# Performance work log

Hardware: AMD Instinct MI355X
Metric: run time of the kernel (lower is better)

## Reference

```python
import jax, jax.numpy as jnp
import numpy as np
from jax import lax
from jax.scipy.special import logsumexp

TEMP_MIN, TEMP_MAX = 0.1, 1.0
B, I, J, C = 2, 128, 512, 256


def setup_inputs() -> dict:
    key = jax.random.key(0)
    k1, k2, k3 = jax.random.split(key, 3)
    return {
        "text_embeddings": jax.random.normal(k1, (B, I, C), dtype=jnp.float32),
        "mel_embeddings": jax.random.normal(k2, (B, J, C), dtype=jnp.float32),
        "text_mask": jnp.ones((B, I), dtype=jnp.float32),
        "mel_mask": jnp.ones((B, J), dtype=jnp.float32),
        "noise": jax.random.gumbel(k3, (B, I, J), dtype=jnp.float32),  # -log(-log(U))
        "temperature_ratio": jnp.float32(0.5),
    }


def _cond_prob(energy, text_mask, mel_mask, direction):
    # energy: [B, I, J]; returns [B, I, J, K] log conditional probs (normalized over axis 2)
    b, i, j = energy.shape
    if direction == "alpha":
        k = j
        tri = jnp.arange(j)[:, None] >= jnp.arange(k)[None, :]  # triu(ones(J,J)).T layout -> j >= k
        mel_k = mel_mask
    else:  # beta
        k = j - 1
        tri = jnp.arange(j)[:, None] <= jnp.arange(k)[None, :]  # tril(ones(J-1,J)).T layout -> j <= k
        mel_k = mel_mask[:, :k]
    valid = (
        (text_mask[:, :, None, None] * mel_mask[:, None, :, None] * mel_k[:, None, None, :]) > 0
    ) & tri[None, None]
    e4 = jnp.where(valid, energy[..., None], -jnp.inf)  # [B,I,J,K]
    e4 = e4 - logsumexp(e4, axis=2, keepdims=True)
    return jnp.where(valid, e4, jnp.asarray(-10.0, energy.dtype))


def reference(text_embeddings, mel_embeddings, text_mask, mel_mask, noise, temperature_ratio):
    b, i_len, ct = text_embeddings.shape
    j_len, cm = mel_embeddings.shape[1], mel_embeddings.shape[2]
    ninf = jnp.asarray(-jnp.inf, text_embeddings.dtype)

    energy = jnp.einsum("bic,bjc->bij", text_embeddings, mel_embeddings) / np.sqrt(ct * cm)
    temperature = TEMP_MIN + (TEMP_MAX - TEMP_MIN) * temperature_ratio
    energy = (energy + noise) / temperature

    cpa = _cond_prob(energy, text_mask, mel_mask, "alpha")  # [B,I,J,J]
    cpb = _cond_prob(energy, text_mask, mel_mask, "beta")   # [B,I,J,J-1]

    # forward (alpha) recursion over text dim: alpha[:, i, j+1] = LSE_k(alpha[:, i-1, k] + cpa[:, i-1, j, k])
    init_a = jnp.full((b, j_len + 1), -jnp.inf, energy.dtype).at[:, 0].set(0.0)

    def astep(carry, cpa_i):  # carry [B, J+1], cpa_i [B, J, J]
        row = logsumexp(carry[:, None, :-1] + cpa_i, axis=2)  # [B, J]
        new = jnp.concatenate([jnp.full((b, 1), -jnp.inf, energy.dtype), row], axis=1)
        return new, row

    _, arows = lax.scan(astep, init_a, jnp.swapaxes(cpa, 0, 1))
    alpha = jnp.swapaxes(arows, 0, 1)  # [B, I, J] == alpha[:, 1:, 1:]

    # backward (beta) recursion: beta[:, i, j] = LSE_k(beta[:, i+1, k+1] + cpb[:, i, j, k])
    init_b = jnp.full((b, j_len), -jnp.inf, energy.dtype).at[:, -1].set(0.0)

    def bstep(carry, cpb_i):  # carry [B, J], cpb_i [B, J, J-1]
        row = logsumexp(carry[:, None, 1:] + cpb_i, axis=2)
        return row, row

    _, brows = lax.scan(bstep, init_b, jnp.flip(jnp.swapaxes(cpb[:, : i_len - 1], 0, 1), axis=0))
    beta = jnp.concatenate([jnp.flip(brows, axis=0), init_b[None]], axis=0)
    beta = jnp.swapaxes(beta, 0, 1)  # [B, I, J]

    gamma = alpha + beta
    gmask = (text_mask[:, :, None] * mel_mask[:, None, :]) > 0
    gamma = jnp.where(gmask, gamma, ninf)
    gamma = jnp.where(gmask, gamma - logsumexp(gamma, axis=1, keepdims=True), ninf)

    expanded = jnp.einsum("bij,bic->bjc", jnp.exp(gamma), text_embeddings)
    expanded = expanded * mel_mask[:, :, None]
    return gamma, expanded
```

## Files before the change

kernel.cpp:

```cpp
#include <hip/hip_runtime.h>
#include <math.h>

#define BB 2
#define II 128
#define JJ 512
#define CC 256
#define NEL (BB*II*JJ)
#define NINF (-INFINITY)
#define K10 4.5399929762484854e-5f

template<int CTRL, int RM = 0xf, int BM = 0xf, bool BC = true>
__device__ __forceinline__ float dppf(float x) {
    return __int_as_float(__builtin_amdgcn_update_dpp(
        0, __float_as_int(x), CTRL, RM, BM, BC));
}
__device__ __forceinline__ float wscan_incl(float x) {
    x += dppf<0x111>(x);
    x += dppf<0x112>(x);
    x += dppf<0x114>(x);
    x += dppf<0x118>(x);
    x += dppf<0x142, 0xa>(x);
    x += dppf<0x143, 0xc>(x);
    return x;
}
__device__ __forceinline__ float lane_shr1(float x) { return dppf<0x138>(x); }
__device__ __forceinline__ float bcast63(float x) {
    return __int_as_float(__builtin_amdgcn_readlane(__float_as_int(x), 63));
}

__device__ __forceinline__ void tree_prefix8(const float x[8], float P[8]) {
    float t[8];
    t[0] = x[0];
    #pragma unroll
    for (int q = 1; q < 8; ++q) t[q] = x[q] + x[q-1];
    float u[8];
    u[0] = t[0]; u[1] = t[1];
    #pragma unroll
    for (int q = 2; q < 8; ++q) u[q] = t[q] + t[q-2];
    P[0] = u[0]; P[1] = u[1]; P[2] = u[2]; P[3] = u[3];
    #pragma unroll
    for (int q = 4; q < 8; ++q) P[q] = u[q] + u[q-4];
}

__device__ __forceinline__ void loadrow8(const float* __restrict__ p, float v[8]) {
    float4 a = *reinterpret_cast<const float4*>(p);
    float4 b = *reinterpret_cast<const float4*>(p + 4);
    v[0]=a.x; v[1]=a.y; v[2]=a.z; v[3]=a.w;
    v[4]=b.x; v[5]=b.y; v[6]=b.z; v[7]=b.w;
}
__device__ __forceinline__ void loadrow8_rev(const float* __restrict__ row, int lane, float v[8]) {
    float t[8];
    loadrow8(row + 504 - 8 * lane, t);
    #pragma unroll
    for (int q = 0; q < 8; ++q) v[q] = t[7 - q];
}
__device__ __forceinline__ void storerow8(float* __restrict__ p, const float v[8]) {
    *reinterpret_cast<float4*>(p)     = make_float4(v[0],v[1],v[2],v[3]);
    *reinterpret_cast<float4*>(p + 4) = make_float4(v[4],v[5],v[6],v[7]);
}

__global__ __launch_bounds__(256) void energy_kernel(
        const float* __restrict__ text, const float* __restrict__ mel,
        const float* __restrict__ noise, const float* __restrict__ ratio,
        float* __restrict__ e) {
    __shared__ float melS[64][65];
    __shared__ float texS[8][65];
    int b  = blockIdx.x;
    int i0 = blockIdx.y * 8;
    int j0 = blockIdx.z * 64;
    int t = threadIdx.x;
    int jj = t & 63, ig = t >> 6;
    float acc0 = 0.f, acc1 = 0.f;
    for (int cc = 0; cc < CC; cc += 64) {
        #pragma unroll
        for (int k = 0; k < 4; ++k) {
            int idx = t + k * 256;
            int row = idx >> 4, seg = idx & 15;
            float4 v = *reinterpret_cast<const float4*>(
                mel + (size_t)(b * JJ + j0 + row) * CC + cc + seg * 4);
            melS[row][seg*4+0] = v.x; melS[row][seg*4+1] = v.y;
            melS[row][seg*4+2] = v.z; melS[row][seg*4+3] = v.w;
        }
        if (t < 128) {
            int row = t >> 4, seg = t & 15;
            float4 v = *reinterpret_cast<const float4*>(
                text + (size_t)(b * II + i0 + row) * CC + cc + seg * 4);
            texS[row][seg*4+0] = v.x; texS[row][seg*4+1] = v.y;
            texS[row][seg*4+2] = v.z; texS[row][seg*4+3] = v.w;
        }
        __syncthreads();
        #pragma unroll 8
        for (int c = 0; c < 64; ++c) {
            float m = melS[jj][c];
            acc0 = fmaf(m, texS[ig*2+0][c], acc0);
            acc1 = fmaf(m, texS[ig*2+1][c], acc1);
        }
        __syncthreads();
    }
    float temp = 0.1f + 0.9f * ratio[0];
    float rtmp = 1.0f / temp;
    int r0 = (b * II + i0 + ig*2 + 0) * JJ + j0 + jj;
    int r1 = (b * II + i0 + ig*2 + 1) * JJ + j0 + jj;
    e[r0] = (acc0 * (1.0f/256.0f) + noise[r0]) * rtmp;
    e[r1] = (acc1 * (1.0f/256.0f) + noise[r1]) * rtmp;
}

__global__ __launch_bounds__(64) void dscan_kernel(
        const float* __restrict__ e, float* __restrict__ Ee,
        float* __restrict__ Wa, float* __restrict__ Wb) {
    int row = blockIdx.x;
    int lane = threadIdx.x;
    float v[8];
    loadrow8(e + row * JJ + lane * 8, v);
    float m = v[0];
    #pragma unroll
    for (int q = 1; q < 8; ++q) m = fmaxf(m, v[q]);
    #pragma unroll
    for (int d = 1; d < 64; d <<= 1) m = fmaxf(m, __shfl_xor(m, d, 64));
    float x[8];
    #pragma unroll
    for (int q = 0; q < 8; ++q) x[q] = __expf(v[q] - m);
    storerow8(Ee + row * JJ + lane * 8, x);
    float run = 0.f, P[8];
    #pragma unroll
    for (int q = 0; q < 8; ++q) { run += x[q]; P[q] = run; }
    float sc = wscan_incl(run);
    float cp = lane_shr1(sc);
    float run2 = 0.f, S[8];
    #pragma unroll
    for (int q = 7; q >= 0; --q) { run2 += x[q]; S[q] = run2; }
    float sd = run2;
    #pragma unroll
    for (int d = 1; d < 64; d <<= 1) { float o = __shfl_down(sd, d, 64); sd += (lane + d < 64) ? o : 0.0f; }
    float cs = __shfl_down(sd, 1, 64); if (lane == 63) cs = 0.f;
    float wa[8], wb[8];
    #pragma unroll
    for (int q = 0; q < 8; ++q) {
        wa[q] = 1.0f / (S[q] + cs);
        wb[q] = 1.0f / (P[q] + cp);
    }
    storerow8(Wa + row * JJ + lane * 8, wa);
    storerow8(Wb + row * JJ + lane * 8, wb);
}

template<bool NORM>
__device__ __forceinline__ void astep(
    int i, int lane, int off, bool pf,
    float (&p)[8], float& c,
    float (&CE)[8], float (&CW)[8],
    float (&LE)[8], float (&LW)[8],
    const float* __restrict__ EeB, const float* __restrict__ WaB,
    float* __restrict__ paB, float* __restrict__ caB)
{
    storerow8(paB + (size_t)(i - 1) * JJ + off, p);
    if (lane == 0) caB[i - 1] = c;
    __builtin_amdgcn_sched_barrier(0);
    if (pf) {
        loadrow8(EeB + (size_t)(i + 3) * JJ + off, LE);
        loadrow8(WaB + (size_t)(i + 3) * JJ + off, LW);
    }
    __builtin_amdgcn_sched_barrier(0);

    float pup = lane_shr1(p[7]);
    float y[8];
    y[0] = pup * CW[0];
    #pragma unroll
    for (int q = 1; q < 8; ++q) y[q] = p[q-1] * CW[q];
    float zz[8];
    #pragma unroll
    for (int q = 0; q < 7; ++q) zz[q] = p[q];
    zz[7] = (lane == 63) ? 0.0f : p[7];
    float Y[8], Z[8];
    tree_prefix8(y, Y);
    tree_prefix8(zz, Z);
    float sy = wscan_incl(Y[7]);
    float sz = wscan_incl(Z[7]);
    float oy = lane_shr1(sy);
    float oz = lane_shr1(sz);
    float T  = bcast63(sz);
    #pragma unroll
    for (int q = 0; q < 8; ++q) {
        float S1 = oy + Y[q];
        float S2 = fmaxf(T - (oz + Z[q]) + zz[q], 0.0f);
        p[q] = fmaf(CE[q], S1, K10 * S2);
    }
    if (NORM) {
        float Tc = fmaxf(T, 1e-30f);
        float rT = __builtin_amdgcn_rcpf(Tc);
        c += __logf(Tc);
        #pragma unroll
        for (int q = 0; q < 8; ++q) p[q] *= rT;
    }
}

template<bool NORM>
__device__ __forceinline__ void bstep(
    int i, int lane, int off, bool pf,
    float (&p)[8], float& c,
    float (&CE)[8], float (&CW)[8],
    float (&LE)[8], float (&LW)[8],
    const float* __restrict__ EeB, const float* __restrict__ WbB,
    float* __restrict__ pbB, float* __restrict__ cbB)
{
    storerow8(pbB + (size_t)(i + 1) * JJ + off, p);
    if (lane == 0) cbB[i + 1] = c;
    __builtin_amdgcn_sched_barrier(0);
    if (pf) {
        loadrow8_rev(EeB + (size_t)(i - 3) * JJ, lane, LE);
        loadrow8_rev(WbB + (size_t)(i - 3) * JJ, lane, LW);
    }
    __builtin_amdgcn_sched_barrier(0);

    float pup = lane_shr1(p[7]);
    float pn[8];
    pn[0] = pup;
    #pragma unroll
    for (int q = 1; q < 8; ++q) pn[q] = p[q-1];
    float w[8];
    #pragma unroll
    for (int q = 0; q < 8; ++q) w[q] = pn[q] * CW[q];
    float W[8], N[8];
    tree_prefix8(w, W);
    tree_prefix8(pn, N);
    float sw = wscan_incl(W[7]);
    float sn = wscan_incl(N[7]);
    float ow = lane_shr1(sw);
    float on = lane_shr1(sn);
    float T  = bcast63(sn);
    #pragma unroll
    for (int q = 0; q < 8; ++q) {
        float QA = ow + W[q];
        float QB = fmaxf(T - (on + N[q]), 0.0f);
        p[q] = fmaf(CE[q], QA, K10 * QB);
    }
    if (NORM) {
        float Tc = fmaxf(T, 1e-30f);
        float rT = __builtin_amdgcn_rcpf(Tc);
        c += __logf(Tc);
        #pragma unroll
        for (int q = 0; q < 8; ++q) p[q] *= rT;
    }
}

__global__ __launch_bounds__(64) void scan_ab_kernel(
        const float* __restrict__ Ee, const float* __restrict__ Wa,
        const float* __restrict__ Wb,
        float* __restrict__ pa, float* __restrict__ pb,
        float* __restrict__ ca, float* __restrict__ cb) {
    int b = blockIdx.x >> 1, dir = blockIdx.x & 1;
    int lane = threadIdx.x, off = lane * 8;
    size_t base = (size_t)b * II * JJ;
    float p[8], c = 0.0f;
    float B0e[8], B0w[8], B1e[8], B1w[8], B2e[8], B2w[8], B3e[8], B3w[8];

    if (dir == 0) {
        const float* EeB = Ee + base; const float* WaB = Wa + base;
        float* paB = pa + base; float* caB = ca + b * II;
        loadrow8(EeB + (size_t)1*JJ + off, B1e); loadrow8(WaB + (size_t)1*JJ + off, B1w);
        loadrow8(EeB + (size_t)2*JJ + off, B2e); loadrow8(WaB + (size_t)2*JJ + off, B2w);
        loadrow8(EeB + (size_t)3*JJ + off, B3e); loadrow8(WaB + (size_t)3*JJ + off, B3w);
        float e0[8];
        loadrow8(EeB + off, e0);
        float wa00 = WaB[0];
        #pragma unroll
        for (int q = 0; q < 8; ++q) p[q] = e0[q] * wa00;
        int i = 1;
        #pragma unroll 1
        for (; i + 3 <= II - 1; i += 4) {
            astep<true >(i,   lane, off, i+3 < II, p, c, B1e,B1w, B0e,B0w, EeB,WaB,paB,caB);
            astep<false>(i+1, lane, off, i+4 < II, p, c, B2e,B2w, B1e,B1w, EeB,WaB,paB,caB);
            astep<false>(i+2, lane, off, i+5 < II, p, c, B3e,B3w, B2e,B2w, EeB,WaB,paB,caB);
            astep<false>(i+3, lane, off, i+6 < II, p, c, B0e,B0w, B3e,B3w, EeB,WaB,paB,caB);
        }
        astep<true >(125, lane, off, false, p, c, B1e,B1w, B0e,B0w, EeB,WaB,paB,caB);
        astep<false>(126, lane, off, false, p, c, B2e,B2w, B1e,B1w, EeB,WaB,paB,caB);
        astep<false>(127, lane, off, false, p, c, B3e,B3w, B2e,B2w, EeB,WaB,paB,caB);
        storerow8(paB + (size_t)127 * JJ + off, p);
        if (lane == 0) caB[127] = c;
    } else {
        const float* EeB = Ee + base; const float* WbB = Wb + base;
        float* pbB = pb + base; float* cbB = cb + b * II;
        loadrow8_rev(EeB + (size_t)126*JJ, lane, B2e); loadrow8_rev(WbB + (size_t)126*JJ, lane, B2w);
        loadrow8_rev(EeB + (size_t)125*JJ, lane, B1e); loadrow8_rev(WbB + (size_t)125*JJ, lane, B1w);
        loadrow8_rev(EeB + (size_t)124*JJ, lane, B0e); loadrow8_rev(WbB + (size_t)124*JJ, lane, B0w);
        #pragma unroll
        for (int q = 0; q < 8; ++q) p[q] = 0.0f;
        p[0] = (lane == 0) ? 1.0f : 0.0f;
        int i = II - 2;
        #pragma unroll 1
        for (; i - 3 >= 0; i -= 4) {
            bstep<true >(i,   lane, off, i-3 >= 0, p, c, B2e,B2w, B3e,B3w, EeB,WbB,pbB,cbB);
            bstep<false>(i-1, lane, off, i-4 >= 0, p, c, B1e,B1w, B2e,B2w, EeB,WbB,pbB,cbB);
            bstep<false>(i-2, lane, off, i-5 >= 0, p, c, B0e,B0w, B1e,B1w, EeB,WbB,pbB,cbB);
            bstep<false>(i-3, lane, off, i-6 >= 0, p, c, B3e,B3w, B0e,B0w, EeB,WbB,pbB,cbB);
        }
        bstep<true >(2, lane, off, false, p, c, B2e,B2w, B3e,B3w, EeB,WbB,pbB,cbB);
        bstep<false>(1, lane, off, false, p, c, B1e,B1w, B2e,B2w, EeB,WbB,pbB,cbB);
        bstep<false>(0, lane, off, false, p, c, B0e,B0w, B1e,B1w, EeB,WbB,pbB,cbB);
        storerow8(pbB + off, p);
        if (lane == 0) cbB[0] = c;
    }
}

__global__ __launch_bounds__(256) void gamma_expand_kernel(
        const float* __restrict__ pa, const float* __restrict__ pb,
        const float* __restrict__ ca, const float* __restrict__ cb,
        const float* __restrict__ text, const float* __restrict__ mmask,
        float* __restrict__ gamma_out, float* __restrict__ expanded) {
    __shared__ float wt[II][9];
    __shared__ float Ei[II];
    __shared__ float red[8][33];
    int b   = blockIdx.x >> 6;
    int jj0 = (blockIdx.x & 63) * 8;
    int t = threadIdx.x;
    int q = t & 7, ic = t >> 3;

    if (t < II) Ei[t] = ca[b*II + t] + cb[b*II + t];
    __syncthreads();
    float maxc = Ei[0];
    #pragma unroll 16
    for (int i = 1; i < II; ++i) maxc = fmaxf(maxc, Ei[i]);
    __syncthreads();
    if (t < II) Ei[t] = __expf(Ei[t] - maxc);
    __syncthreads();

    size_t idx0  = (size_t)b * II * JJ + jj0 + q;
    size_t idx0r = (size_t)b * II * JJ + (JJ - 1 - jj0 - q);
    float d = 0.f;
    #pragma unroll
    for (int k = 0; k < 4; ++k) {
        int i = ic * 4 + k;
        float P = pa[idx0 + (size_t)i * JJ] * pb[idx0r + (size_t)i * JJ] * Ei[i];
        wt[i][q] = P;
        d += P;
    }
    red[q][ic] = d;
    __syncthreads();
    if (t < 8) {
        float s = 0.f;
        #pragma unroll
        for (int k = 0; k < 32; ++k) s += red[t][k];
        red[t][32] = 1.0f / fmaxf(s, 1e-37f);
    }
    __syncthreads();
    float rD = red[q][32];
    #pragma unroll
    for (int k = 0; k < 4; ++k) {
        int i = ic * 4 + k;
        float P = wt[i][q] * rD;
        wt[i][q] = P;
        gamma_out[idx0 + (size_t)i * JJ] = fmaxf(__logf(P), -1e30f);
    }
    __syncthreads();

    float acc[8] = {0,0,0,0,0,0,0,0};
    const float* txb = text + (size_t)b * II * CC + t;
    #pragma unroll 4
    for (int i = 0; i < II; ++i) {
        float tv = txb[(size_t)i * CC];
        #pragma unroll
        for (int qq = 0; qq < 8; ++qq) acc[qq] = fmaf(wt[i][qq], tv, acc[qq]);
    }
    #pragma unroll
    for (int qq = 0; qq < 8; ++qq) {
        expanded[(size_t)(b * JJ + jj0 + qq) * CC + t] =
            acc[qq] * mmask[b * JJ + jj0 + qq];
    }
}

extern "C" void kernel_launch(void* const* d_in, const int* in_sizes, int n_in,
                              void* d_out, int out_size, void* d_ws, size_t ws_size,
                              hipStream_t stream) {
    const float* text  = (const float*)d_in[0];
    const float* mel   = (const float*)d_in[1];
    const float* mmask = (const float*)d_in[3];
    const float* noise = (const float*)d_in[4];
    const float* ratio = (const float*)d_in[5];
    float* gamma_out = (float*)d_out;
    float* expanded  = (float*)d_out + NEL;

    float* ws = (float*)d_ws;
    float* Ee = ws;
    float* Wa = ws +   NEL;
    float* Wb = ws + 2*NEL;
    float* pa = ws + 3*NEL;
    float* pb = ws + 4*NEL;
    float* ca = ws + 5*NEL;
    float* cb = ws + 5*NEL + BB*II;
    float* e  = pa;

    hipLaunchKernelGGL(energy_kernel, dim3(BB, II/8, JJ/64), dim3(256), 0, stream,
                       text, mel, noise, ratio, e);
    hipLaunchKernelGGL(dscan_kernel, dim3(BB*II), dim3(64), 0, stream, e, Ee, Wa, Wb);
    hipLaunchKernelGGL(scan_ab_kernel, dim3(BB*2), dim3(64), 0, stream,
                       Ee, Wa, Wb, pa, pb, ca, cb);
    hipLaunchKernelGGL(gamma_expand_kernel, dim3(BB*64), dim3(256), 0, stream,
                       pa, pb, ca, cb, text, mmask, gamma_out, expanded);
}
```

Baseline: 141.8 us.

## Spread alpha/beta scan rows across 8 waves with LDS cross-wave prefix

The sequential alpha/beta recursion kernel moves from one 64-lane wave holding 8 elements per lane to a 512-thread block with one element per thread. Each step does an in-wave DPP scan, then combines the 8 wave totals through a small double-buffered LDS array behind one barrier per step. Prefetch depth grows to 8 rows, issued as hand-written asm loads with explicit vmcnt waits, and the normalisation constants are staged in LDS. The aim is to shorten the serial per-step latency by spreading work over more lanes. In exchange every one of the 127 steps now pays an LDS round trip and a workgroup barrier.

New measurement: 156.7 us. +10.5%, slower.

```diff
diff --git a/kernel.cpp b/kernel.cpp
--- a/kernel.cpp
+++ b/kernel.cpp
@@ -8,6 +8,8 @@
 #define NEL (BB*II*JJ)
 #define NINF (-INFINITY)
 #define K10 4.5399929762484854e-5f
+
+typedef float f32x4 __attribute__((ext_vector_type(4)));
 
 template<int CTRL, int RM = 0xf, int BM = 0xf, bool BC = true>
 __device__ __forceinline__ float dppf(float x) {
@@ -24,9 +26,6 @@
     return x;
 }
 __device__ __forceinline__ float lane_shr1(float x) { return dppf<0x138>(x); }
-__device__ __forceinline__ float bcast63(float x) {
-    return __int_as_float(__builtin_amdgcn_readlane(__float_as_int(x), 63));
-}
 
 __device__ __forceinline__ void tree_prefix8(const float x[8], float P[8]) {
     float t[8];
@@ -42,21 +41,30 @@
     for (int q = 4; q < 8; ++q) P[q] = u[q] + u[q-4];
 }
 
-__device__ __forceinline__ void loadrow8(const float* __restrict__ p, float v[8]) {
+__device__ __forceinline__ void loadrow8(const float* p, float v[8]) {
     float4 a = *reinterpret_cast<const float4*>(p);
     float4 b = *reinterpret_cast<const float4*>(p + 4);
     v[0]=a.x; v[1]=a.y; v[2]=a.z; v[3]=a.w;
     v[4]=b.x; v[5]=b.y; v[6]=b.z; v[7]=b.w;
 }
-__device__ __forceinline__ void loadrow8_rev(const float* __restrict__ row, int lane, float v[8]) {
-    float t[8];
-    loadrow8(row + 504 - 8 * lane, t);
-    #pragma unroll
-    for (int q = 0; q < 8; ++q) v[q] = t[7 - q];
-}
 __device__ __forceinline__ void storerow8(float* __restrict__ p, const float v[8]) {
     *reinterpret_cast<float4*>(p)     = make_float4(v[0],v[1],v[2],v[3]);
     *reinterpret_cast<float4*>(p + 4) = make_float4(v[4],v[5],v[6],v[7]);
+}
+
+__device__ __forceinline__ void aload1(float &d, const float* p) {
+    asm volatile("global_load_dword %0, %1, off" : "=&v"(d) : "v"(p) : "memory");
+}
+__device__ __forceinline__ void astore1(float d, float* p) {
+    asm volatile("global_store_dword %1, %0, off" :: "v"(d), "v"(p) : "memory");
+}
+template<int N> __device__ __forceinline__ void waitcnt_vm() {
+    asm volatile("s_waitcnt vmcnt(%0)" :: "i"(N) : "memory");
+}
+__device__ __forceinline__ void lgkm0_barrier() {
+    asm volatile("s_waitcnt lgkmcnt(0)" ::: "memory");
+    __builtin_amdgcn_s_barrier();
+    __builtin_amdgcn_sched_barrier(0);
 }
 
 __global__ __launch_bounds__(256) void energy_kernel(
@@ -143,162 +151,200 @@
     storerow8(Wb + row * JJ + lane * 8, wb);
 }
 
-template<bool NORM>
-__device__ __forceinline__ void astep(
-    int i, int lane, int off, bool pf,
-    float (&p)[8], float& c,
-    float (&CE)[8], float (&CW)[8],
-    float (&LE)[8], float (&LW)[8],
+
+template<bool NORM, int VM, bool PF, int PTY>
+__device__ __forceinline__ void astep8(int i, int t, int w, int lane,
+    float pin, float &pout, float &c, float &Be, float &Bw,
     const float* __restrict__ EeB, const float* __restrict__ WaB,
-    float* __restrict__ paB, float* __restrict__ caB)
+    float* __restrict__ paB, f32x4 (*ldsX)[8], float* ldsC)
 {
-    storerow8(paB + (size_t)(i - 1) * JJ + off, p);
-    if (lane == 0) caB[i - 1] = c;
+    astore1(pin, paB + (size_t)(i - 1) * JJ + t);
+    if (t == 0) ldsC[i - 1] = c;
+    waitcnt_vm<VM>();
     __builtin_amdgcn_sched_barrier(0);
-    if (pf) {
-        loadrow8(EeB + (size_t)(i + 3) * JJ + off, LE);
-        loadrow8(WaB + (size_t)(i + 3) * JJ + off, LW);
-    }
-    __builtin_amdgcn_sched_barrier(0);
-
-    float pup = lane_shr1(p[7]);
-    float y[8];
-    y[0] = pup * CW[0];
-    #pragma unroll
-    for (int q = 1; q < 8; ++q) y[q] = p[q-1] * CW[q];
-    float zz[8];
-    #pragma unroll
-    for (int q = 0; q < 7; ++q) zz[q] = p[q];
-    zz[7] = (lane == 63) ? 0.0f : p[7];
-    float Y[8], Z[8];
-    tree_prefix8(y, Y);
-    tree_prefix8(zz, Z);
-    float sy = wscan_incl(Y[7]);
-    float sz = wscan_incl(Z[7]);
-    float oy = lane_shr1(sy);
-    float oz = lane_shr1(sz);
-    float T  = bcast63(sz);
-    #pragma unroll
-    for (int q = 0; q < 8; ++q) {
-        float S1 = oy + Y[q];
-        float S2 = fmaxf(T - (oz + Z[q]) + zz[q], 0.0f);
-        p[q] = fmaf(CE[q], S1, K10 * S2);
-    }
+    float CE = Be, CW = Bw;
+    if (PF) { aload1(Be, EeB + (size_t)(i + 8) * JJ + t);
+              aload1(Bw, WaB + (size_t)(i + 8) * JJ + t); }
+    float zz   = (t == JJ - 1) ? 0.0f : pin;
+    float y_in = lane_shr1(pin) * CW;
+    float Yl_in = wscan_incl(y_in);
+    float Zl    = wscan_incl(zz);
+    float cw0 = __int_as_float(__builtin_amdgcn_readlane(__float_as_int(CW), 0));
+    if (lane == 63) { f32x4 xv = {pin, Yl_in, Zl, cw0}; ldsX[PTY][w] = xv; }
+    lgkm0_barrier();
+    float offY = 0.f, offZ = 0.f, T = 0.f, prevP = 0.f, pupw = 0.f;
+    #pragma unroll
+    for (int v = 0; v < 8; ++v) {
+        f32x4 xv = ldsX[PTY][v];
+        float pup_v = prevP;
+        float tY = fmaf(pup_v, xv[3], xv[1]);
+        float tZ = xv[2];
+        if (v < w)  { offY += tY; offZ += tZ; }
+        if (v == w) pupw = pup_v;
+        T += tZ;
+        prevP = xv[0];
+    }
+    float S1 = offY + Yl_in + pupw * cw0;
+    float S2 = fmaxf(T - (offZ + Zl) + zz, 0.0f);
+    pout = fmaf(CE, S1, K10 * S2);
     if (NORM) {
         float Tc = fmaxf(T, 1e-30f);
         float rT = __builtin_amdgcn_rcpf(Tc);
         c += __logf(Tc);
-        #pragma unroll
-        for (int q = 0; q < 8; ++q) p[q] *= rT;
-    }
-}
-
-template<bool NORM>
-__device__ __forceinline__ void bstep(
-    int i, int lane, int off, bool pf,
-    float (&p)[8], float& c,
-    float (&CE)[8], float (&CW)[8],
-    float (&LE)[8], float (&LW)[8],
+        pout *= rT;
+    }
+}
+
+template<bool NORM, int VM, bool PF, int PTY>
+__device__ __forceinline__ void bstep8(int i, int t, int w, int lane,
+    float pin, float &pout, float &c, float &Be, float &Bw,
     const float* __restrict__ EeB, const float* __restrict__ WbB,
-    float* __restrict__ pbB, float* __restrict__ cbB)
+    float* __restrict__ pbB, f32x4 (*ldsX)[8], float* ldsC)
 {
-    storerow8(pbB + (size_t)(i + 1) * JJ + off, p);
-    if (lane == 0) cbB[i + 1] = c;
+    astore1(pin, pbB + (size_t)(i + 1) * JJ + t);
+    if (t == 0) ldsC[i + 1] = c;
+    waitcnt_vm<VM>();
     __builtin_amdgcn_sched_barrier(0);
-    if (pf) {
-        loadrow8_rev(EeB + (size_t)(i - 3) * JJ, lane, LE);
-        loadrow8_rev(WbB + (size_t)(i - 3) * JJ, lane, LW);
-    }
-    __builtin_amdgcn_sched_barrier(0);
-
-    float pup = lane_shr1(p[7]);
-    float pn[8];
-    pn[0] = pup;
-    #pragma unroll
-    for (int q = 1; q < 8; ++q) pn[q] = p[q-1];
-    float w[8];
-    #pragma unroll
-    for (int q = 0; q < 8; ++q) w[q] = pn[q] * CW[q];
-    float W[8], N[8];
-    tree_prefix8(w, W);
-    tree_prefix8(pn, N);
-    float sw = wscan_incl(W[7]);
-    float sn = wscan_incl(N[7]);
-    float ow = lane_shr1(sw);
-    float on = lane_shr1(sn);
-    float T  = bcast63(sn);
-    #pragma unroll
-    for (int q = 0; q < 8; ++q) {
-        float QA = ow + W[q];
-        float QB = fmaxf(T - (on + N[q]), 0.0f);
-        p[q] = fmaf(CE[q], QA, K10 * QB);
-    }
+    float CE = Be, CW = Bw;
+    if (PF) { aload1(Be, EeB + (size_t)(i - 8) * JJ + (JJ - 1 - t));
+              aload1(Bw, WbB + (size_t)(i - 8) * JJ + (JJ - 1 - t)); }
+    float pn_in = lane_shr1(pin);
+    float w_in  = pn_in * CW;
+    float Wl_in = wscan_incl(w_in);
+    float Nl_in = wscan_incl(pn_in);
+    float cw0 = __int_as_float(__builtin_amdgcn_readlane(__float_as_int(CW), 0));
+    if (lane == 63) { f32x4 xv = {pin, Wl_in, Nl_in, cw0}; ldsX[PTY][w] = xv; }
+    lgkm0_barrier();
+    float offW = 0.f, offN = 0.f, T = 0.f, prevP = 0.f, pupw = 0.f;
+    #pragma unroll
+    for (int v = 0; v < 8; ++v) {
+        f32x4 xv = ldsX[PTY][v];
+        float pup_v = prevP;
+        float tW = fmaf(pup_v, xv[3], xv[1]);
+        float tN = xv[2] + pup_v;
+        if (v < w)  { offW += tW; offN += tN; }
+        if (v == w) pupw = pup_v;
+        T += tN;
+        prevP = xv[0];
+    }
+    float QA = offW + Wl_in + pupw * cw0;
+    float Nl = Nl_in + pupw;
+    float QB = fmaxf(T - (offN + Nl), 0.0f);
+    pout = fmaf(CE, QA, K10 * QB);
     if (NORM) {
         float Tc = fmaxf(T, 1e-30f);
         float rT = __builtin_amdgcn_rcpf(Tc);
         c += __logf(Tc);
-        #pragma unroll
-        for (int q = 0; q < 8; ++q) p[q] *= rT;
-    }
-}
-
-__global__ __launch_bounds__(64) void scan_ab_kernel(
+        pout *= rT;
+    }
+}
+
+__global__ __launch_bounds__(512, 1) void scan_ab_kernel(
         const float* __restrict__ Ee, const float* __restrict__ Wa,
         const float* __restrict__ Wb,
         float* __restrict__ pa, float* __restrict__ pb,
         float* __restrict__ ca, float* __restrict__ cb) {
+    __shared__ f32x4 ldsX[2][8];
+    __shared__ float ldsC[II];
     int b = blockIdx.x >> 1, dir = blockIdx.x & 1;
-    int lane = threadIdx.x, off = lane * 8;
+    int t = threadIdx.x;
+    int w = t >> 6, lane = t & 63;
     size_t base = (size_t)b * II * JJ;
-    float p[8], c = 0.0f;
-    float B0e[8], B0w[8], B1e[8], B1w[8], B2e[8], B2w[8], B3e[8], B3w[8];
+    float P0, P1, P2, P3, c = 0.0f;
+    float S0e,S0w,S1e,S1w,S2e,S2w,S3e,S3w,S4e,S4w,S5e,S5w,S6e,S6w,S7e,S7w;
 
     if (dir == 0) {
         const float* EeB = Ee + base; const float* WaB = Wa + base;
         float* paB = pa + base; float* caB = ca + b * II;
-        loadrow8(EeB + (size_t)1*JJ + off, B1e); loadrow8(WaB + (size_t)1*JJ + off, B1w);
-        loadrow8(EeB + (size_t)2*JJ + off, B2e); loadrow8(WaB + (size_t)2*JJ + off, B2w);
-        loadrow8(EeB + (size_t)3*JJ + off, B3e); loadrow8(WaB + (size_t)3*JJ + off, B3w);
-        float e0[8];
-        loadrow8(EeB + off, e0);
+        float e0 = EeB[t];
         float wa00 = WaB[0];
-        #pragma unroll
-        for (int q = 0; q < 8; ++q) p[q] = e0[q] * wa00;
-        int i = 1;
+        P0 = e0 * wa00;
+        __builtin_amdgcn_sched_barrier(0);
+        aload1(S1e, EeB + (size_t)1*JJ + t); aload1(S1w, WaB + (size_t)1*JJ + t);
+        aload1(S2e, EeB + (size_t)2*JJ + t); aload1(S2w, WaB + (size_t)2*JJ + t);
+        aload1(S3e, EeB + (size_t)3*JJ + t); aload1(S3w, WaB + (size_t)3*JJ + t);
+        aload1(S4e, EeB + (size_t)4*JJ + t); aload1(S4w, WaB + (size_t)4*JJ + t);
+        aload1(S5e, EeB + (size_t)5*JJ + t); aload1(S5w, WaB + (size_t)5*JJ + t);
+        aload1(S6e, EeB + (size_t)6*JJ + t); aload1(S6w, WaB + (size_t)6*JJ + t);
+        aload1(S7e, EeB + (size_t)7*JJ + t); aload1(S7w, WaB + (size_t)7*JJ + t);
+        aload1(S0e, EeB + (size_t)8*JJ + t); aload1(S0w, WaB + (size_t)8*JJ + t);
+        astep8<true ,15,true,1>(1, t,w,lane, P0, P1, c, S1e,S1w, EeB,WaB,paB, ldsX, ldsC);
+        astep8<false,16,true,0>(2, t,w,lane, P1, P2, c, S2e,S2w, EeB,WaB,paB, ldsX, ldsC);
+        astep8<false,17,true,1>(3, t,w,lane, P2, P3, c, S3e,S3w, EeB,WaB,paB, ldsX, ldsC);
+        astep8<false,18,true,0>(4, t,w,lane, P3, P0, c, S4e,S4w, EeB,WaB,paB, ldsX, ldsC);
+        astep8<true ,19,true,1>(5, t,w,lane, P0, P1, c, S5e,S5w, EeB,WaB,paB, ldsX, ldsC);
+        astep8<false,20,true,0>(6, t,w,lane, P1, P2, c, S6e,S6w, EeB,WaB,paB, ldsX, ldsC);
+        astep8<false,21,true,1>(7, t,w,lane, P2, P3, c, S7e,S7w, EeB,WaB,paB, ldsX, ldsC);
         #pragma unroll 1
-        for (; i + 3 <= II - 1; i += 4) {
-            astep<true >(i,   lane, off, i+3 < II, p, c, B1e,B1w, B0e,B0w, EeB,WaB,paB,caB);
-            astep<false>(i+1, lane, off, i+4 < II, p, c, B2e,B2w, B1e,B1w, EeB,WaB,paB,caB);
-            astep<false>(i+2, lane, off, i+5 < II, p, c, B3e,B3w, B2e,B2w, EeB,WaB,paB,caB);
-            astep<false>(i+3, lane, off, i+6 < II, p, c, B0e,B0w, B3e,B3w, EeB,WaB,paB,caB);
+        for (int d = 0; d < 14; ++d) {
+            int i = 8 + 8 * d;
+            astep8<false,22,true,0>(i+0, t,w,lane, P3, P0, c, S0e,S0w, EeB,WaB,paB, ldsX, ldsC);
+            astep8<true ,22,true,1>(i+1, t,w,lane, P0, P1, c, S1e,S1w, EeB,WaB,paB, ldsX, ldsC);
+            astep8<false,22,true,0>(i+2, t,w,lane, P1, P2, c, S2e,S2w, EeB,WaB,paB, ldsX, ldsC);
+            astep8<false,22,true,1>(i+3, t,w,lane, P2, P3, c, S3e,S3w, EeB,WaB,paB, ldsX, ldsC);
+            astep8<false,22,true,0>(i+4, t,w,lane, P3, P0, c, S4e,S4w, EeB,WaB,paB, ldsX, ldsC);
+            astep8<true ,22,true,1>(i+5, t,w,lane, P0, P1, c, S5e,S5w, EeB,WaB,paB, ldsX, ldsC);
+            astep8<false,22,true,0>(i+6, t,w,lane, P1, P2, c, S6e,S6w, EeB,WaB,paB, ldsX, ldsC);
+            astep8<false,22,true,1>(i+7, t,w,lane, P2, P3, c, S7e,S7w, EeB,WaB,paB, ldsX, ldsC);
         }
-        astep<true >(125, lane, off, false, p, c, B1e,B1w, B0e,B0w, EeB,WaB,paB,caB);
-        astep<false>(126, lane, off, false, p, c, B2e,B2w, B1e,B1w, EeB,WaB,paB,caB);
-        astep<false>(127, lane, off, false, p, c, B3e,B3w, B2e,B2w, EeB,WaB,paB,caB);
-        storerow8(paB + (size_t)127 * JJ + off, p);
-        if (lane == 0) caB[127] = c;
+        astep8<false,22,false,0>(120, t,w,lane, P3, P0, c, S0e,S0w, EeB,WaB,paB, ldsX, ldsC);
+        astep8<true ,20,false,1>(121, t,w,lane, P0, P1, c, S1e,S1w, EeB,WaB,paB, ldsX, ldsC);
+        astep8<false,18,false,0>(122, t,w,lane, P1, P2, c, S2e,S2w, EeB,WaB,paB, ldsX, ldsC);
+        astep8<false,16,false,1>(123, t,w,lane, P2, P3, c, S3e,S3w, EeB,WaB,paB, ldsX, ldsC);
+        astep8<false,14,false,0>(124, t,w,lane, P3, P0, c, S4e,S4w, EeB,WaB,paB, ldsX, ldsC);
+        astep8<true ,12,false,1>(125, t,w,lane, P0, P1, c, S5e,S5w, EeB,WaB,paB, ldsX, ldsC);
+        astep8<false,10,false,0>(126, t,w,lane, P1, P2, c, S6e,S6w, EeB,WaB,paB, ldsX, ldsC);
+        astep8<false, 8,false,1>(127, t,w,lane, P2, P3, c, S7e,S7w, EeB,WaB,paB, ldsX, ldsC);
+        astore1(P3, paB + (size_t)127 * JJ + t);
+        if (t == 0) ldsC[127] = c;
+        waitcnt_vm<0>();
+        lgkm0_barrier();
+        if (t < II) caB[t] = ldsC[t];
     } else {
         const float* EeB = Ee + base; const float* WbB = Wb + base;
         float* pbB = pb + base; float* cbB = cb + b * II;
-        loadrow8_rev(EeB + (size_t)126*JJ, lane, B2e); loadrow8_rev(WbB + (size_t)126*JJ, lane, B2w);
-        loadrow8_rev(EeB + (size_t)125*JJ, lane, B1e); loadrow8_rev(WbB + (size_t)125*JJ, lane, B1w);
-        loadrow8_rev(EeB + (size_t)124*JJ, lane, B0e); loadrow8_rev(WbB + (size_t)124*JJ, lane, B0w);
-        #pragma unroll
-        for (int q = 0; q < 8; ++q) p[q] = 0.0f;
-        p[0] = (lane == 0) ? 1.0f : 0.0f;
-        int i = II - 2;
+        P0 = (t == 0) ? 1.0f : 0.0f;
+        __builtin_amdgcn_sched_barrier(0);
+        aload1(S6e, EeB + (size_t)126*JJ + (JJ-1-t)); aload1(S6w, WbB + (size_t)126*JJ + (JJ-1-t));
+        aload1(S5e, EeB + (size_t)125*JJ + (JJ-1-t)); aload1(S5w, WbB + (size_t)125*JJ + (JJ-1-t));
+        aload1(S4e, EeB + (size_t)124*JJ + (JJ-1-t)); aload1(S4w, WbB + (size_t)124*JJ + (JJ-1-t));
+        aload1(S3e, EeB + (size_t)123*JJ + (JJ-1-t)); aload1(S3w, WbB + (size_t)123*JJ + (JJ-1-t));
+        aload1(S2e, EeB + (size_t)122*JJ + (JJ-1-t)); aload1(S2w, WbB + (size_t)122*JJ + (JJ-1-t));
+        aload1(S1e, EeB + (size_t)121*JJ + (JJ-1-t)); aload1(S1w, WbB + (size_t)121*JJ + (JJ-1-t));
+        aload1(S0e, EeB + (size_t)120*JJ + (JJ-1-t)); aload1(S0w, WbB + (size_t)120*JJ + (JJ-1-t));
+        aload1(S7e, EeB + (size_t)119*JJ + (JJ-1-t)); aload1(S7w, WbB + (size_t)119*JJ + (JJ-1-t));
+        bstep8<true ,15,true,0>(126, t,w,lane, P0, P1, c, S6e,S6w, EeB,WbB,pbB, ldsX, ldsC);
+        bstep8<false,16,true,1>(125, t,w,lane, P1, P2, c, S5e,S5w, EeB,WbB,pbB, ldsX, ldsC);
+        bstep8<false,17,true,0>(124, t,w,lane, P2, P3, c, S4e,S4w, EeB,WbB,pbB, ldsX, ldsC);
+        bstep8<false,18,true,1>(123, t,w,lane, P3, P0, c, S3e,S3w, EeB,WbB,pbB, ldsX, ldsC);
+        bstep8<true ,19,true,0>(122, t,w,lane, P0, P1, c, S2e,S2w, EeB,WbB,pbB, ldsX, ldsC);
+        bstep8<false,20,true,1>(121, t,w,lane, P1, P2, c, S1e,S1w, EeB,WbB,pbB, ldsX, ldsC);
+        bstep8<false,21,true,0>(120, t,w,lane, P2, P3, c, S0e,S0w, EeB,WbB,pbB, ldsX, ldsC);
         #pragma unroll 1
-        for (; i - 3 >= 0; i -= 4) {
-            bstep<true >(i,   lane, off, i-3 >= 0, p, c, B2e,B2w, B3e,B3w, EeB,WbB,pbB,cbB);
-            bstep<false>(i-1, lane, off, i-4 >= 0, p, c, B1e,B1w, B2e,B2w, EeB,WbB,pbB,cbB);
-            bstep<false>(i-2, lane, off, i-5 >= 0, p, c, B0e,B0w, B1e,B1w, EeB,WbB,pbB,cbB);
-            bstep<false>(i-3, lane, off, i-6 >= 0, p, c, B3e,B3w, B0e,B0w, EeB,WbB,pbB,cbB);
+        for (int d = 0; d < 14; ++d) {
+            int i = 119 - 8 * d;
+            bstep8<false,22,true,1>(i-0, t,w,lane, P3, P0, c, S7e,S7w, EeB,WbB,pbB, ldsX, ldsC);
+            bstep8<true ,22,true,0>(i-1, t,w,lane, P0, P1, c, S6e,S6w, EeB,WbB,pbB, ldsX, ldsC);
+            bstep8<false,22,true,1>(i-2, t,w,lane, P1, P2, c, S5e,S5w, EeB,WbB,pbB, ldsX, ldsC);
+            bstep8<false,22,true,0>(i-3, t,w,lane, P2, P3, c, S4e,S4w, EeB,WbB,pbB, ldsX, ldsC);
+            bstep8<false,22,true,1>(i-4, t,w,lane, P3, P0, c, S3e,S3w, EeB,WbB,pbB, ldsX, ldsC);
+            bstep8<true ,22,true,0>(i-5, t,w,lane, P0, P1, c, S2e,S2w, EeB,WbB,pbB, ldsX, ldsC);
+            bstep8<false,22,true,1>(i-6, t,w,lane, P1, P2, c, S1e,S1w, EeB,WbB,pbB, ldsX, ldsC);
+            bstep8<false,22,true,0>(i-7, t,w,lane, P2, P3, c, S0e,S0w, EeB,WbB,pbB, ldsX, ldsC);
         }
-        bstep<true >(2, lane, off, false, p, c, B2e,B2w, B3e,B3w, EeB,WbB,pbB,cbB);
-        bstep<false>(1, lane, off, false, p, c, B1e,B1w, B2e,B2w, EeB,WbB,pbB,cbB);
-        bstep<false>(0, lane, off, false, p, c, B0e,B0w, B1e,B1w, EeB,WbB,pbB,cbB);
-        storerow8(pbB + off, p);
-        if (lane == 0) cbB[0] = c;
+        bstep8<false,22,false,1>(7, t,w,lane, P3, P0, c, S7e,S7w, EeB,WbB,pbB, ldsX, ldsC);
+        bstep8<true ,20,false,0>(6, t,w,lane, P0, P1, c, S6e,S6w, EeB,WbB,pbB, ldsX, ldsC);
+        bstep8<false,18,false,1>(5, t,w,lane, P1, P2, c, S5e,S5w, EeB,WbB,pbB, ldsX, ldsC);
+        bstep8<false,16,false,0>(4, t,w,lane, P2, P3, c, S4e,S4w, EeB,WbB,pbB, ldsX, ldsC);
+        bstep8<false,14,false,1>(3, t,w,lane, P3, P0, c, S3e,S3w, EeB,WbB,pbB, ldsX, ldsC);
+        bstep8<true ,12,false,0>(2, t,w,lane, P0, P1, c, S2e,S2w, EeB,WbB,pbB, ldsX, ldsC);
+        bstep8<false,10,false,1>(1, t,w,lane, P1, P2, c, S1e,S1w, EeB,WbB,pbB, ldsX, ldsC);
+        bstep8<false, 8,false,0>(0, t,w,lane, P2, P3, c, S0e,S0w, EeB,WbB,pbB, ldsX, ldsC);
+        astore1(P3, pbB + t);
+        if (t == 0) ldsC[0] = c;
+        waitcnt_vm<0>();
+        lgkm0_barrier();
+        if (t < II) cbB[t] = ldsC[t];
     }
 }
 
@@ -392,7 +438,7 @@
     hipLaunchKernelGGL(energy_kernel, dim3(BB, II/8, JJ/64), dim3(256), 0, stream,
                        text, mel, noise, ratio, e);
     hipLaunchKernelGGL(dscan_kernel, dim3(BB*II), dim3(64), 0, stream, e, Ee, Wa, Wb);
-    hipLaunchKernelGGL(scan_ab_kernel, dim3(BB*2), dim3(64), 0, stream,
+    hipLaunchKernelGGL(scan_ab_kernel, dim3(BB*2), dim3(512), 0, stream,
                        Ee, Wa, Wb, pa, pb, ca, cb);
     hipLaunchKernelGGL(gamma_expand_kernel, dim3(BB*64), dim3(256), 0, stream,
                        pa, pb, ca, cb, text, mmask, gamma_out, expanded);
```
